# Kernel tuning notes

Measured on AMD Instinct MI355X. Metric: run time of the kernel, lower is better.

The kernel has to match this reference:

```python
import jax, jax.numpy as jnp
import numpy as np

B, S, D, F, R = 4, 2048, 2048, 8192, 16


def setup_inputs() -> dict:
    key = jax.random.key(0)
    ks = jax.random.split(key, 13)
    sc = 0.02  # weight scale to keep activations well-conditioned
    return {
        "x1": jax.random.normal(ks[0], (B, S, D), jnp.float32),
        "w_gate": jax.random.normal(ks[1], (D, F), jnp.float32) * sc,
        "b_gate": jax.random.normal(ks[2], (F,), jnp.float32) * sc,
        "w_gate_lora_a": jax.random.normal(ks[3], (D, R), jnp.float32) * sc,
        "w_gate_lora_b": jax.random.normal(ks[4], (R, F), jnp.float32) * sc,
        "w_up": jax.random.normal(ks[5], (D, F), jnp.float32) * sc,
        "b_up": jax.random.normal(ks[6], (F,), jnp.float32) * sc,
        "w_up_lora_a": jax.random.normal(ks[7], (D, R), jnp.float32) * sc,
        "w_up_lora_b": jax.random.normal(ks[8], (R, F), jnp.float32) * sc,
        "w_down": jax.random.normal(ks[9], (F, D), jnp.float32) * sc,
        "b_down": jax.random.normal(ks[10], (D,), jnp.float32) * sc,
        "w_down_lora_a": jax.random.normal(ks[11], (F, R), jnp.float32) * sc,
        "w_down_lora_b": jax.random.normal(ks[12], (R, D), jnp.float32) * sc,
    }


def reference(x1, w_gate, b_gate, w_gate_lora_a, w_gate_lora_b,
              w_up, b_up, w_up_lora_a, w_up_lora_b,
              w_down, b_down, w_down_lora_a, w_down_lora_b):
    # gate projection: dequantized base GEMM + bias + rank-R LoRA
    y1 = x1 @ w_gate + b_gate + (x1 @ w_gate_lora_a) @ w_gate_lora_b  # [B,S,F]
    # up projection
    y2 = x1 @ w_up + b_up + (x1 @ w_up_lora_a) @ w_up_lora_b          # [B,S,F]
    # activation_forward == 'relu' gated product
    x3 = jax.nn.relu(y1) * y2                                          # [B,S,F]
    # down projection
    y3 = x3 @ w_down + b_down + (x3 @ w_down_lora_a) @ w_down_lora_b  # [B,S,D]
    return y3
```

## Files before the change

kernel.cpp:

```cpp
#include <hip/hip_runtime.h>

typedef __bf16 bf16x8 __attribute__((ext_vector_type(8)));
typedef float f32x4 __attribute__((ext_vector_type(4)));

#define MFMA16(a, b, c) __builtin_amdgcn_mfma_f32_16x16x32_bf16((a), (b), (c), 0, 0, 0)

__device__ __forceinline__ unsigned short f2bf(float f) {
    unsigned int u = __float_as_uint(f);
    u += 0x7fffu + ((u >> 16) & 1u);
    return (unsigned short)(u >> 16);
}

__device__ __forceinline__ void gload16(const unsigned short* g, unsigned short* l) {
    __builtin_amdgcn_global_load_lds(
        (__attribute__((address_space(1))) void*)(void*)g,
        (__attribute__((address_space(3))) void*)(void*)l,
        16, 0, 0);
}


__device__ __forceinline__ void ld_frag4(const unsigned short* base, int w0, int h,
                                         int l16, int quad, bf16x8* f) {
#pragma unroll
    for (int i = 0; i < 4; ++i) {
        const int r = w0 + i * 16 + l16;
        f[i] = *(const bf16x8*)(base + r * 64 + (((h * 4 + quad) ^ (r & 7)) * 8));
    }
}

__device__ __forceinline__ void mfma16x(const bf16x8* af, const bf16x8* bf, f32x4 (*acc)[4]) {
    __builtin_amdgcn_s_setprio(1);
#pragma unroll
    for (int i = 0; i < 4; ++i)
#pragma unroll
        for (int j = 0; j < 4; ++j) acc[i][j] = MFMA16(af[i], bf[j], acc[i][j]);
    __builtin_amdgcn_s_setprio(0);
}

#define ASM_VMCNT2 asm volatile("s_waitcnt vmcnt(2)" ::: "memory")
#define ASM_VMCNT0 asm volatile("s_waitcnt vmcnt(0)" ::: "memory")
#define ASM_LGKM0  asm volatile("s_waitcnt lgkmcnt(0)" ::: "memory")

__global__ void cast_x_kernel(const float4* __restrict__ x, ushort4* __restrict__ xb) {
    const size_t i = (size_t)blockIdx.x * 256 + threadIdx.x;
    const float4 v = x[i];
    ushort4 o;
    o.x = f2bf(v.x); o.y = f2bf(v.y); o.z = f2bf(v.z); o.w = f2bf(v.w);
    xb[i] = o;
}

__global__ void prep_wT(const float* __restrict__ W, const float* __restrict__ A,
                        const float* __restrict__ B2, unsigned short* __restrict__ WT,
                        const int K, const int N) {
    __shared__ float tile[64][65];
    __shared__ float As[64][16];
    __shared__ float Bs[16][64];
    const int t = threadIdx.x;
    const int k0 = blockIdx.x * 64;
    const int n0 = blockIdx.y * 64;

    for (int i = t; i < 64 * 16; i += 256)
        As[i >> 4][i & 15] = A[(size_t)(k0 + (i >> 4)) * 16 + (i & 15)];
    for (int i = t; i < 16 * 64; i += 256)
        Bs[i >> 6][i & 63] = B2[(size_t)(i >> 6) * N + n0 + (i & 63)];
    __syncthreads();

    const int c = t & 63;
    const int r0 = t >> 6;
    for (int rr = 0; rr < 64; rr += 4) {
        const int r = rr + r0;
        float v = W[(size_t)(k0 + r) * N + n0 + c];
#pragma unroll
        for (int q = 0; q < 16; ++q) v += As[r][q] * Bs[q][c];
        tile[r][c] = v;
    }
    __syncthreads();
    for (int rr = 0; rr < 64; rr += 4) {
        const int r = rr + r0;
        WT[(size_t)(n0 + r) * K + k0 + c] = f2bf(tile[c][r]);
    }
}

__global__ __launch_bounds__(512, 2)
void gemm_gateup(const unsigned short* __restrict__ Xb,
                 const unsigned short* __restrict__ WgT,
                 const unsigned short* __restrict__ WuT,
                 const float* __restrict__ bg, const float* __restrict__ bu,
                 unsigned short* __restrict__ X3) {
    constexpr int K = 2048, F = 8192, BK = 64, NT = K / BK;
    extern __shared__ __align__(16) unsigned short lds[];
    unsigned short* const A0 = lds;
    unsigned short* const G0 = lds + 32768;
    unsigned short* const U0 = lds + 49152;

    const int tid = threadIdx.x;
    const int lane = tid & 63;
    const int wave = tid >> 6;
    const int wm = (wave >> 1) * 64;
    const int wn = (wave & 1) * 64;
    const int l16 = lane & 15;
    const int quad = lane >> 4;

    const int m0 = blockIdx.x * 256;
    const int n0 = blockIdx.y * 128;

    const unsigned short* Ag = Xb + (size_t)m0 * K;
    const unsigned short* Gg = WgT + (size_t)n0 * K;
    const unsigned short* Ug = WuT + (size_t)n0 * K;

    int srow[2], soff[2];
#pragma unroll
    for (int j = 0; j < 2; ++j) {
        const int c = tid + j * 512;
        srow[j] = c >> 3;
        soff[j] = ((c & 7) ^ (srow[j] & 7)) * 8;
    }
    const int dst0 = tid * 8, dst1 = (tid + 512) * 8;

#define STAGE(gptr, lbase, kk, roff)                                                        \
    do {                                                                                    \
        gload16((gptr) + (size_t)(srow[0] + (roff)) * K + (kk) + soff[0], (lbase) + dst0);  \
        gload16((gptr) + (size_t)(srow[1] + (roff)) * K + (kk) + soff[1], (lbase) + dst1);  \
    } while (0)

    f32x4 accg[4][4] = {};
    f32x4 accu[4][4] = {};
    bf16x8 af[4], bfr[4];

    STAGE(Ag, A0, 0, 0);
    STAGE(Ag, A0 + 8192, 0, 128);
    STAGE(Gg, G0, 0, 0);
    STAGE(Ug, U0, 0, 0);
    ASM_VMCNT2;
    __builtin_amdgcn_s_barrier();
    __builtin_amdgcn_sched_barrier(0);

    for (int t = 0; t < NT; ++t) {
        const int p = t & 1, q = p ^ 1;
        const unsigned short* Ap = A0 + p * 16384;
        const unsigned short* Gp = G0 + p * 8192;
        const unsigned short* Up = U0 + p * 8192;
        unsigned short* const Aq = A0 + q * 16384;
        unsigned short* const Gq = G0 + q * 8192;
        unsigned short* const Uq = U0 + q * 8192;
        const int kn = (t + 1) * BK;
        const bool pf = (t + 1 < NT);

        ld_frag4(Ap, wm, 0, l16, quad, af);
        ld_frag4(Gp, wn, 0, l16, quad, bfr);
        if (pf) STAGE(Ag, Aq, kn, 0);
        __builtin_amdgcn_s_barrier();
        ASM_LGKM0;
        __builtin_amdgcn_sched_barrier(0);
        mfma16x(af, bfr, accg);
        if (pf) {
            ASM_VMCNT2;
        } else {
            ASM_VMCNT0;
        }
        __builtin_amdgcn_s_barrier();
        __builtin_amdgcn_sched_barrier(0);

        ld_frag4(Up, wn, 0, l16, quad, bfr);
        if (pf) STAGE(Ag, Aq + 8192, kn, 128);
        __builtin_amdgcn_s_barrier();
        ASM_LGKM0;
        __builtin_amdgcn_sched_barrier(0);
        mfma16x(af, bfr, accu);
        __builtin_amdgcn_s_barrier();

        ld_frag4(Ap, wm, 1, l16, quad, af);
        ld_frag4(Gp, wn, 1, l16, quad, bfr);
        if (pf) STAGE(Gg, Gq, kn, 0);
        __builtin_amdgcn_s_barrier();
        ASM_LGKM0;
        __builtin_amdgcn_sched_barrier(0);
        mfma16x(af, bfr, accg);
        __builtin_amdgcn_s_barrier();

        ld_frag4(Up, wn, 1, l16, quad, bfr);
        if (pf) STAGE(Ug, Uq, kn, 0);
        __builtin_amdgcn_s_barrier();
        ASM_LGKM0;
        __builtin_amdgcn_sched_barrier(0);
        mfma16x(af, bfr, accu);
        ASM_VMCNT2;
        __builtin_amdgcn_s_barrier();
        __builtin_amdgcn_sched_barrier(0);
    }
#undef STAGE

#pragma unroll
    for (int j = 0; j < 4; ++j) {
        const int col = n0 + wn + j * 16 + l16;
        const float bgv = bg[col];
        const float buv = bu[col];
#pragma unroll
        for (int i = 0; i < 4; ++i) {
            const int rowb = m0 + wm + i * 16 + quad * 4;
#pragma unroll
            for (int r = 0; r < 4; ++r) {
                float g = accg[i][j][r] + bgv;
                float u = accu[i][j][r] + buv;
                g = g > 0.f ? g : 0.f;
                X3[(size_t)(rowb + r) * F + col] = f2bf(g * u);
            }
        }
    }
}

__global__ __launch_bounds__(256, 3)
void gemm_down(const unsigned short* __restrict__ X3,
               const unsigned short* __restrict__ WdT,
               const float* __restrict__ bd, float* __restrict__ out) {
    constexpr int K = 8192, N = 2048;
    constexpr int BK = 64;
    __shared__ __align__(16) unsigned short As[128 * BK];
    __shared__ __align__(16) unsigned short Bs[128 * BK];

    const int tid = threadIdx.x;
    const int lane = tid & 63;
    const int wave = tid >> 6;
    const int wm = (wave >> 1) * 64;
    const int wn = (wave & 1) * 64;
    const int l16 = lane & 15;
    const int quad = lane >> 4;

    const int m0 = blockIdx.x * 128;
    const int n0 = blockIdx.y * 128;

    const unsigned short* Ag = X3 + (size_t)m0 * K;
    const unsigned short* Bgp = WdT + (size_t)n0 * K;

    int srow[4], soff[4];
#pragma unroll
    for (int j = 0; j < 4; ++j) {
        const int c = tid + j * 256;
        srow[j] = c >> 3;
        soff[j] = ((c & 7) ^ (srow[j] & 7)) * 8;
    }

    f32x4 acc[4][4] = {};

    for (int k0 = 0; k0 < K; k0 += BK) {
#pragma unroll
        for (int j = 0; j < 4; ++j)
            gload16(Ag + (size_t)srow[j] * K + k0 + soff[j], As + (tid + j * 256) * 8);
#pragma unroll
        for (int j = 0; j < 4; ++j)
            gload16(Bgp + (size_t)srow[j] * K + k0 + soff[j], Bs + (tid + j * 256) * 8);
        __syncthreads();
#pragma unroll
        for (int h = 0; h < 2; ++h) {
            bf16x8 af[4], bfr[4];
#pragma unroll
            for (int i = 0; i < 4; ++i) {
                const int ra = wm + i * 16 + l16;
                const int rb = wn + i * 16 + l16;
                const int pa = ((h * 4 + quad) ^ (ra & 7)) * 8;
                const int pb = ((h * 4 + quad) ^ (rb & 7)) * 8;
                af[i] = *(const bf16x8*)(As + ra * BK + pa);
                bfr[i] = *(const bf16x8*)(Bs + rb * BK + pb);
            }
#pragma unroll
            for (int i = 0; i < 4; ++i)
#pragma unroll
                for (int j = 0; j < 4; ++j)
                    acc[i][j] = MFMA16(af[i], bfr[j], acc[i][j]);
        }
        __syncthreads();
    }

#pragma unroll
    for (int j = 0; j < 4; ++j) {
        const int col = n0 + wn + j * 16 + l16;
        const float bdv = bd[col];
#pragma unroll
        for (int i = 0; i < 4; ++i) {
            const int rowb = m0 + wm + i * 16 + quad * 4;
#pragma unroll
            for (int r = 0; r < 4; ++r)
                out[(size_t)(rowb + r) * N + col] = acc[i][j][r] + bdv;
        }
    }
}

extern "C" void kernel_launch(void* const* d_in, const int* in_sizes, int n_in,
                              void* d_out, int out_size, void* d_ws, size_t ws_size,
                              hipStream_t stream) {
    const float* x1      = (const float*)d_in[0];
    const float* w_gate  = (const float*)d_in[1];
    const float* b_gate  = (const float*)d_in[2];
    const float* a_gate  = (const float*)d_in[3];
    const float* lb_gate = (const float*)d_in[4];
    const float* w_up    = (const float*)d_in[5];
    const float* b_up    = (const float*)d_in[6];
    const float* a_up    = (const float*)d_in[7];
    const float* lb_up   = (const float*)d_in[8];
    const float* w_down  = (const float*)d_in[9];
    const float* b_down  = (const float*)d_in[10];
    const float* a_down  = (const float*)d_in[11];
    const float* lb_down = (const float*)d_in[12];

    constexpr int M = 8192, D = 2048, F = 8192;

    static bool attr_set = false;
    if (!attr_set) {
        (void)hipFuncSetAttribute((const void*)gemm_gateup,
                                  hipFuncAttributeMaxDynamicSharedMemorySize, 131072);
        attr_set = true;
    }

    char* ws = (char*)d_ws;
    unsigned short* Xb  = (unsigned short*)ws;
    unsigned short* WgT = (unsigned short*)(ws + 33554432ULL);
    unsigned short* WuT = (unsigned short*)(ws + 67108864ULL);
    unsigned short* WdT = (unsigned short*)(ws + 100663296ULL);
    unsigned short* X3  = (unsigned short*)(ws + 134217728ULL);

    cast_x_kernel<<<dim3((M * D) / 4 / 256), dim3(256), 0, stream>>>(
        (const float4*)x1, (ushort4*)Xb);
    prep_wT<<<dim3(D / 64, F / 64), dim3(256), 0, stream>>>(w_gate, a_gate, lb_gate, WgT, D, F);
    prep_wT<<<dim3(D / 64, F / 64), dim3(256), 0, stream>>>(w_up, a_up, lb_up, WuT, D, F);
    prep_wT<<<dim3(F / 64, D / 64), dim3(256), 0, stream>>>(w_down, a_down, lb_down, WdT, F, D);

    gemm_gateup<<<dim3(M / 256, F / 128), dim3(512), 131072, stream>>>(
        Xb, WgT, WuT, b_gate, b_up, X3);
    gemm_down<<<dim3(M / 128, D / 128), dim3(256), 0, stream>>>(
        X3, WdT, b_down, (float*)d_out);
}
```

Measured before the change: 1.049 ms.

## Triple-buffer down-projection GEMM with 256x128 tiles and async LDS prefetch

Rewrites gemm_down to use 512-thread blocks with 256x128 output tiles and a three-stage LDS ring buffer in dynamic shared memory. Global-to-LDS loads for step t+2 are issued while MFMAs run on step t, with vmcnt waits and raw s_barriers replacing the full __syncthreads around each K step. This aims to hide global load latency and get more B-tile reuse. In exchange it uses 144KB of LDS per block, so at most one block fits per CU, and the barrier and waitcnt sequencing is harder to get right.

```diff
diff --git a/kernel.cpp b/kernel.cpp
--- a/kernel.cpp
+++ b/kernel.cpp
@@ -37,6 +37,7 @@
     __builtin_amdgcn_s_setprio(0);
 }
 
+#define ASM_VMCNT6 asm volatile("s_waitcnt vmcnt(6)" ::: "memory")
 #define ASM_VMCNT2 asm volatile("s_waitcnt vmcnt(2)" ::: "memory")
 #define ASM_VMCNT0 asm volatile("s_waitcnt vmcnt(0)" ::: "memory")
 #define ASM_LGKM0  asm volatile("s_waitcnt lgkmcnt(0)" ::: "memory")
@@ -209,14 +210,14 @@
     }
 }
 
-__global__ __launch_bounds__(256, 3)
+__global__ __launch_bounds__(512, 2)
 void gemm_down(const unsigned short* __restrict__ X3,
                const unsigned short* __restrict__ WdT,
                const float* __restrict__ bd, float* __restrict__ out) {
-    constexpr int K = 8192, N = 2048;
-    constexpr int BK = 64;
-    __shared__ __align__(16) unsigned short As[128 * BK];
-    __shared__ __align__(16) unsigned short Bs[128 * BK];
+    constexpr int K = 8192, N = 2048, BK = 64, NT = K / BK;
+    extern __shared__ __align__(16) unsigned short lds[];
+#define ABUF(b) (lds + (b) * 24576)
+#define BBUF(b) (lds + (b) * 24576 + 16384)
 
     const int tid = threadIdx.x;
     const int lane = tid & 63;
@@ -226,50 +227,77 @@
     const int l16 = lane & 15;
     const int quad = lane >> 4;
 
-    const int m0 = blockIdx.x * 128;
+    const int m0 = blockIdx.x * 256;
     const int n0 = blockIdx.y * 128;
 
     const unsigned short* Ag = X3 + (size_t)m0 * K;
-    const unsigned short* Bgp = WdT + (size_t)n0 * K;
-
-    int srow[4], soff[4];
-#pragma unroll
-    for (int j = 0; j < 4; ++j) {
-        const int c = tid + j * 256;
+    const unsigned short* Bg = WdT + (size_t)n0 * K;
+
+    int srow[2], soff[2];
+#pragma unroll
+    for (int j = 0; j < 2; ++j) {
+        const int c = tid + j * 512;
         srow[j] = c >> 3;
         soff[j] = ((c & 7) ^ (srow[j] & 7)) * 8;
     }
+    const int dst0 = tid * 8, dst1 = (tid + 512) * 8;
+
+#define STAGE(gptr, lbase, kk, roff)                                                        \
+    do {                                                                                    \
+        gload16((gptr) + (size_t)(srow[0] + (roff)) * K + (kk) + soff[0], (lbase) + dst0);  \
+        gload16((gptr) + (size_t)(srow[1] + (roff)) * K + (kk) + soff[1], (lbase) + dst1);  \
+    } while (0)
 
     f32x4 acc[4][4] = {};
-
-    for (int k0 = 0; k0 < K; k0 += BK) {
-#pragma unroll
-        for (int j = 0; j < 4; ++j)
-            gload16(Ag + (size_t)srow[j] * K + k0 + soff[j], As + (tid + j * 256) * 8);
-#pragma unroll
-        for (int j = 0; j < 4; ++j)
-            gload16(Bgp + (size_t)srow[j] * K + k0 + soff[j], Bs + (tid + j * 256) * 8);
-        __syncthreads();
-#pragma unroll
-        for (int h = 0; h < 2; ++h) {
-            bf16x8 af[4], bfr[4];
-#pragma unroll
-            for (int i = 0; i < 4; ++i) {
-                const int ra = wm + i * 16 + l16;
-                const int rb = wn + i * 16 + l16;
-                const int pa = ((h * 4 + quad) ^ (ra & 7)) * 8;
-                const int pb = ((h * 4 + quad) ^ (rb & 7)) * 8;
-                af[i] = *(const bf16x8*)(As + ra * BK + pa);
-                bfr[i] = *(const bf16x8*)(Bs + rb * BK + pb);
-            }
-#pragma unroll
-            for (int i = 0; i < 4; ++i)
-#pragma unroll
-                for (int j = 0; j < 4; ++j)
-                    acc[i][j] = MFMA16(af[i], bfr[j], acc[i][j]);
-        }
-        __syncthreads();
-    }
+    bf16x8 af[4], bfr[4];
+
+    STAGE(Ag, ABUF(0), 0, 0);
+    STAGE(Ag, ABUF(0) + 8192, 0, 128);
+    STAGE(Bg, BBUF(0), 0, 0);
+    STAGE(Ag, ABUF(1), BK, 0);
+    STAGE(Ag, ABUF(1) + 8192, BK, 128);
+    STAGE(Bg, BBUF(1), BK, 0);
+    ASM_VMCNT6;
+    __builtin_amdgcn_s_barrier();
+    __builtin_amdgcn_sched_barrier(0);
+
+    for (int t = 0; t < NT; ++t) {
+        const unsigned short* Ap = ABUF(t % 3);
+        const unsigned short* Bp = BBUF(t % 3);
+        const int qb = (t + 2) % 3;
+        const int kn = (t + 2) * BK;
+        const bool pf = (t + 2 < NT);
+
+        ld_frag4(Ap, wm, 0, l16, quad, af);
+        ld_frag4(Bp, wn, 0, l16, quad, bfr);
+        if (pf) {
+            STAGE(Ag, ABUF(qb), kn, 0);
+            STAGE(Ag, ABUF(qb) + 8192, kn, 128);
+        }
+        __builtin_amdgcn_s_barrier();
+        ASM_LGKM0;
+        __builtin_amdgcn_sched_barrier(0);
+        mfma16x(af, bfr, acc);
+        __builtin_amdgcn_s_barrier();
+
+        ld_frag4(Ap, wm, 1, l16, quad, af);
+        ld_frag4(Bp, wn, 1, l16, quad, bfr);
+        if (pf) STAGE(Bg, BBUF(qb), kn, 0);
+        __builtin_amdgcn_s_barrier();
+        ASM_LGKM0;
+        __builtin_amdgcn_sched_barrier(0);
+        mfma16x(af, bfr, acc);
+        if (pf) {
+            ASM_VMCNT6;
+        } else {
+            ASM_VMCNT0;
+        }
+        __builtin_amdgcn_s_barrier();
+        __builtin_amdgcn_sched_barrier(0);
+    }
+#undef STAGE
+#undef ABUF
+#undef BBUF
 
 #pragma unroll
     for (int j = 0; j < 4; ++j) {
@@ -308,6 +336,8 @@
     if (!attr_set) {
         (void)hipFuncSetAttribute((const void*)gemm_gateup,
                                   hipFuncAttributeMaxDynamicSharedMemorySize, 131072);
+        (void)hipFuncSetAttribute((const void*)gemm_down,
+                                  hipFuncAttributeMaxDynamicSharedMemorySize, 147456);
         attr_set = true;
     }
 
@@ -326,6 +356,6 @@
 
     gemm_gateup<<<dim3(M / 256, F / 128), dim3(512), 131072, stream>>>(
         Xb, WgT, WuT, b_gate, b_up, X3);
-    gemm_down<<<dim3(M / 128, D / 128), dim3(256), 0, stream>>>(
+    gemm_down<<<dim3(M / 256, D / 128), dim3(512), 147456, stream>>>(
         X3, WdT, b_down, (float*)d_out);
 }
```

Measured after the change: 1.011 ms. -3.6%, faster.
